# Performance work log

Hardware: AMD Instinct MI355X
Metric: run time of the kernel (lower is better)

The kernel has to match this reference:

```python
import jax, jax.numpy as jnp
import numpy as np

B, L, D_INNER, D_STATE, DT_RANK = 1, 1024, 5120, 16, 160


def setup_inputs() -> dict:
    key = jax.random.key(0)
    k0, k1, k2, k3, k4, k5 = jax.random.split(key, 6)
    x = jax.random.normal(k0, (B, L, D_INNER), dtype=jnp.float32)
    # A_log in [0,1) -> A = -exp(A_log) in [-e,-1]: stable decaying recurrence
    A_log = jax.random.uniform(k1, (D_INNER, D_STATE), dtype=jnp.float32)
    D = jax.random.normal(k2, (D_INNER,), dtype=jnp.float32)
    x_proj_w = jax.random.normal(k3, (DT_RANK + 2 * D_STATE, D_INNER), dtype=jnp.float32) * 0.02
    dt_proj_w = jax.random.normal(k4, (D_INNER, DT_RANK), dtype=jnp.float32) * 0.02
    dt_proj_b = jax.random.normal(k5, (D_INNER,), dtype=jnp.float32) * 0.02
    return {"x": x, "A_log": A_log, "D": D, "x_proj_w": x_proj_w,
            "dt_proj_w": dt_proj_w, "dt_proj_b": dt_proj_b}


def reference(x, A_log, D, x_proj_w, dt_proj_w, dt_proj_b):
    # Mamba ssm(): x (b, l, d_inner) -> y (b, l, d_inner)
    A = -jnp.exp(A_log)                                   # (d, n)
    x_dbl = jnp.einsum('bld,ed->ble', x, x_proj_w)        # (b, l, dt_rank+2n)
    dt = x_dbl[..., :DT_RANK]                             # (b, l, r)
    Bm = x_dbl[..., DT_RANK:DT_RANK + D_STATE]            # (b, l, n)
    Cm = x_dbl[..., DT_RANK + D_STATE:]                   # (b, l, n)
    delta = jax.nn.softplus(jnp.einsum('blr,dr->bld', dt, dt_proj_w) + dt_proj_b)

    # discretization (zero-order hold)
    deltaA = jnp.exp(jnp.einsum('bld,dn->bldn', delta, A))        # (b, l, d, n)
    deltaB_u = jnp.einsum('bld,bln,bld->bldn', delta, Bm, x)      # (b, l, d, n)

    def step(h, inp):
        dA_t, dBu_t, c_t = inp          # (b,d,n), (b,d,n), (b,n)
        h = dA_t * h + dBu_t
        y_t = jnp.einsum('bdn,bn->bd', h, c_t)
        return h, y_t

    h0 = jnp.zeros((x.shape[0], D_INNER, D_STATE), dtype=x.dtype)
    xs = (jnp.swapaxes(deltaA, 0, 1),   # (l, b, d, n)
          jnp.swapaxes(deltaB_u, 0, 1),
          jnp.swapaxes(Cm, 0, 1))
    _, ys = jax.lax.scan(step, h0, xs)  # ys: (l, b, d)
    y = jnp.swapaxes(ys, 0, 1)          # (b, l, d)
    return y + x * D
```

## Files before the change

### kernel.cpp

```cpp
#include <hip/hip_runtime.h>
#include <hip/hip_bf16.h>

#define L_SEQ 1024
#define DI    5120
#define DS    16
#define DR    160
#define NE    192
#define NC    16
#define CL    64
#define SPLITK 8
#define KSPLIT (DI / SPLITK)

#define OFF_P     0
#define SZ_P      (SPLITK * L_SEQ * NE * 4)
#define OFF_XDBL  (OFF_P + SZ_P)
#define SZ_XDBL   (L_SEQ * NE * 4)
#define OFF_DELTA (OFF_XDBL + SZ_XDBL)
#define SZ_DELTA  (L_SEQ * DI * 4)
#define OFF_HEND  (OFF_DELTA + SZ_DELTA)
#define SZ_H      (NC * DS * DI * 4)
#define OFF_APROD (OFF_HEND + SZ_H)
#define OFF_WH    OFF_HEND
#define OFF_WL    (OFF_WH + 1638400)
#define OFF_XH    (OFF_WL + 1638400)
#define OFF_XL    (OFF_XH + 393216)

typedef short s16x8 __attribute__((ext_vector_type(8)));
typedef float f32x4 __attribute__((ext_vector_type(4)));

__device__ __forceinline__ unsigned short bf_rn(float f) {
  unsigned u = __float_as_uint(f);
  u += 0x7FFFu + ((u >> 16) & 1u);
  return (unsigned short)(u >> 16);
}
__device__ __forceinline__ void split_hilo(float f, unsigned short& h, unsigned short& l) {
  h = bf_rn(f);
  float hf = __uint_as_float(((unsigned)h) << 16);
  l = bf_rn(f - hf);
}

__device__ __forceinline__ void load_hilo(const float* __restrict__ p,
                                          s16x8& hi, s16x8& lo) {
  float4 v0 = *(const float4*)p;
  float4 v1 = *(const float4*)(p + 4);
  float f[8] = {v0.x, v0.y, v0.z, v0.w, v1.x, v1.y, v1.z, v1.w};
#pragma unroll
  for (int j = 0; j < 8; ++j) {
    unsigned short h, l;
    split_hilo(f[j], h, l);
    hi[j] = (short)h;
    lo[j] = (short)l;
  }
}

__global__ __launch_bounds__(256) void k_cvt(const float* __restrict__ src,
                                             unsigned short* __restrict__ hi,
                                             unsigned short* __restrict__ lo) {
  int i4 = (blockIdx.x * 256 + threadIdx.x) * 4;
  float4 v = *(const float4*)&src[i4];
  float f[4] = {v.x, v.y, v.z, v.w};
  ushort4 h, l;
  unsigned short hh, ll;
  split_hilo(f[0], hh, ll); h.x = hh; l.x = ll;
  split_hilo(f[1], hh, ll); h.y = hh; l.y = ll;
  split_hilo(f[2], hh, ll); h.z = hh; l.z = ll;
  split_hilo(f[3], hh, ll); h.w = hh; l.w = ll;
  *(ushort4*)&hi[i4] = h;
  *(ushort4*)&lo[i4] = l;
}

__global__ __launch_bounds__(128) void k_xdbl_mfma(const float* __restrict__ x,
                                                   const float* __restrict__ xw,
                                                   float* __restrict__ part) {
  const int lane = threadIdx.x & 63;
  const int w    = threadIdx.x >> 6;
  const int e0   = blockIdx.x * 64 + w * 32;
  const int l0   = blockIdx.y * 32;
  const int kb   = blockIdx.z * KSPLIT;
  const int rc   = lane & 15;
  const int kg   = (lane >> 4) * 8;

  f32x4 acc[2][2] = {};
  for (int k0 = 0; k0 < KSPLIT; k0 += 32) {
    s16x8 ahi[2], alo[2], bhi[2], blo[2];
#pragma unroll
    for (int mf = 0; mf < 2; ++mf)
      load_hilo(&x[(size_t)(l0 + mf * 16 + rc) * DI + kb + k0 + kg], ahi[mf], alo[mf]);
#pragma unroll
    for (int nf = 0; nf < 2; ++nf)
      load_hilo(&xw[(size_t)(e0 + nf * 16 + rc) * DI + kb + k0 + kg], bhi[nf], blo[nf]);
#pragma unroll
    for (int mf = 0; mf < 2; ++mf)
#pragma unroll
      for (int nf = 0; nf < 2; ++nf) {
        acc[mf][nf] = __builtin_amdgcn_mfma_f32_16x16x32_bf16(ahi[mf], bhi[nf], acc[mf][nf], 0, 0, 0);
        acc[mf][nf] = __builtin_amdgcn_mfma_f32_16x16x32_bf16(ahi[mf], blo[nf], acc[mf][nf], 0, 0, 0);
        acc[mf][nf] = __builtin_amdgcn_mfma_f32_16x16x32_bf16(alo[mf], bhi[nf], acc[mf][nf], 0, 0, 0);
      }
  }
#pragma unroll
  for (int mf = 0; mf < 2; ++mf)
#pragma unroll
    for (int nf = 0; nf < 2; ++nf)
#pragma unroll
      for (int r = 0; r < 4; ++r) {
        int l = l0 + mf * 16 + (lane >> 4) * 4 + r;
        int e = e0 + nf * 16 + rc;
        part[((size_t)blockIdx.z * L_SEQ + l) * NE + e] = acc[mf][nf][r];
      }
}

__global__ __launch_bounds__(256) void k_xdbl_reduce(const float* __restrict__ part,
                                                     float* __restrict__ xdbl,
                                                     unsigned short* __restrict__ xh,
                                                     unsigned short* __restrict__ xl) {
  int i4 = (blockIdx.x * 256 + threadIdx.x) * 4;
  float4 s = {0.f, 0.f, 0.f, 0.f};
#pragma unroll
  for (int z = 0; z < SPLITK; ++z) {
    float4 p = *(const float4*)&part[(size_t)z * L_SEQ * NE + i4];
    s.x += p.x; s.y += p.y; s.z += p.z; s.w += p.w;
  }
  *(float4*)&xdbl[i4] = s;
  float f[4] = {s.x, s.y, s.z, s.w};
  ushort4 h, l;
  unsigned short hh, ll;
  split_hilo(f[0], hh, ll); h.x = hh; l.x = ll;
  split_hilo(f[1], hh, ll); h.y = hh; l.y = ll;
  split_hilo(f[2], hh, ll); h.z = hh; l.z = ll;
  split_hilo(f[3], hh, ll); h.w = hh; l.w = ll;
  *(ushort4*)&xh[i4] = h;
  *(ushort4*)&xl[i4] = l;
}

#define AST 168
__global__ __launch_bounds__(512) void k_delta_mfma2(const unsigned short* __restrict__ xh,
                                                     const unsigned short* __restrict__ xl,
                                                     const unsigned short* __restrict__ wh,
                                                     const unsigned short* __restrict__ wlo,
                                                     const float* __restrict__ dtb,
                                                     float* __restrict__ delta) {
  __shared__ unsigned short sAh[64 * AST];
  __shared__ unsigned short sAl[64 * AST];
  const int tid  = threadIdx.x;
  const int lane = tid & 63;
  const int w    = tid >> 6;
  const int wl_  = w >> 2;
  const int wd   = w & 3;
  const int l0   = blockIdx.y * 64;
  const int d0   = blockIdx.x * 128 + wd * 32;
  const int rc   = lane & 15;
  const int kg   = (lane >> 4) * 8;

  for (int idx = tid; idx < 64 * 20; idx += 512) {
    int r = idx / 20, c8 = (idx % 20) * 8;
    *(s16x8*)&sAh[r * AST + c8] = *(const s16x8*)&xh[(size_t)(l0 + r) * NE + c8];
    *(s16x8*)&sAl[r * AST + c8] = *(const s16x8*)&xl[(size_t)(l0 + r) * NE + c8];
  }
  __syncthreads();

  f32x4 acc[2][2] = {};
#pragma unroll
  for (int k0 = 0; k0 < DR; k0 += 32) {
    s16x8 ah[2], al[2], bh[2], bl[2];
#pragma unroll
    for (int mf = 0; mf < 2; ++mf) {
      int row = wl_ * 32 + mf * 16 + rc;
      ah[mf] = *(const s16x8*)&sAh[row * AST + k0 + kg];
      al[mf] = *(const s16x8*)&sAl[row * AST + k0 + kg];
    }
#pragma unroll
    for (int nf = 0; nf < 2; ++nf) {
      size_t d = d0 + nf * 16 + rc;
      bh[nf] = *(const s16x8*)&wh[d * DR + k0 + kg];
      bl[nf] = *(const s16x8*)&wlo[d * DR + k0 + kg];
    }
#pragma unroll
    for (int mf = 0; mf < 2; ++mf)
#pragma unroll
      for (int nf = 0; nf < 2; ++nf) {
        acc[mf][nf] = __builtin_amdgcn_mfma_f32_16x16x32_bf16(ah[mf], bh[nf], acc[mf][nf], 0, 0, 0);
        acc[mf][nf] = __builtin_amdgcn_mfma_f32_16x16x32_bf16(ah[mf], bl[nf], acc[mf][nf], 0, 0, 0);
        acc[mf][nf] = __builtin_amdgcn_mfma_f32_16x16x32_bf16(al[mf], bh[nf], acc[mf][nf], 0, 0, 0);
      }
  }
#pragma unroll
  for (int nf = 0; nf < 2; ++nf) {
    int d = d0 + nf * 16 + rc;
    float bias = dtb[d];
#pragma unroll
    for (int mf = 0; mf < 2; ++mf)
#pragma unroll
      for (int r = 0; r < 4; ++r) {
        int l = l0 + wl_ * 32 + mf * 16 + (lane >> 4) * 4 + r;
        float z = acc[mf][nf][r] + bias;
        float sp = fmaxf(z, 0.f) + __logf(1.f + __expf(-fabsf(z)));
        delta[(size_t)l * DI + d] = sp;
      }
  }
}

__global__ __launch_bounds__(256) void k_scan1(const float* __restrict__ x,
                                               const float* __restrict__ delta,
                                               const float* __restrict__ xdbl,
                                               const float* __restrict__ A_log,
                                               float* __restrict__ hend,
                                               float* __restrict__ aprod) {
  const int lane = threadIdx.x & 63;
  const int w    = threadIdx.x >> 6;
  const int d    = blockIdx.x * 64 + w * 16 + (lane & 15);
  const int ng   = lane >> 4;
  const int c    = blockIdx.y;
  __shared__ __align__(16) float sB[CL][DS];
  for (int i = threadIdx.x; i < CL * DS; i += 256) {
    int t = i >> 4, n = i & 15;
    sB[t][n] = xdbl[(size_t)(c * CL + t) * NE + DR + n];
  }
  __syncthreads();
  float4 av = *(const float4*)&A_log[(size_t)d * DS + ng * 4];
  float a[4] = {-__expf(av.x), -__expf(av.y), -__expf(av.z), -__expf(av.w)};
  float h[4] = {0.f, 0.f, 0.f, 0.f};
  float sdl = 0.f;

  const float* dp = &delta[(size_t)(c * CL) * DI + d];
  const float* xp = &x[(size_t)(c * CL) * DI + d];
  float dl = dp[0], xv = xp[0];
#pragma unroll 4
  for (int tt = 0; tt < CL; ++tt) {
    float dl_n = 0.f, xv_n = 0.f;
    if (tt + 1 < CL) { dl_n = dp[(size_t)(tt + 1) * DI]; xv_n = xp[(size_t)(tt + 1) * DI]; }
    float du = dl * xv;
    sdl += dl;
    float4 b4 = *(const float4*)&sB[tt][ng * 4];
    float bb[4] = {b4.x, b4.y, b4.z, b4.w};
#pragma unroll
    for (int j = 0; j < 4; ++j) {
      float dA = __expf(dl * a[j]);
      h[j] = dA * h[j] + du * bb[j];
    }
    dl = dl_n; xv = xv_n;
  }
#pragma unroll
  for (int j = 0; j < 4; ++j) {
    int n = ng * 4 + j;
    hend[(size_t)(c * DS + n) * DI + d] = h[j];
    aprod[(size_t)(c * DS + n) * DI + d] = __expf(a[j] * sdl);
  }
}

__global__ __launch_bounds__(256) void k_scan2(float* __restrict__ hend,
                                               const float* __restrict__ aprod) {
  int i = blockIdx.x * 256 + threadIdx.x;
  float carry = 0.f;
#pragma unroll
  for (int c = 0; c < NC; ++c) {
    size_t idx = (size_t)c * DS * DI + i;
    float apv = aprod[idx];
    float hv = hend[idx];
    hend[idx] = carry;
    carry = apv * carry + hv;
  }
}

__global__ __launch_bounds__(256) void k_scan3(const float* __restrict__ x,
                                               const float* __restrict__ delta,
                                               const float* __restrict__ xdbl,
                                               const float* __restrict__ A_log,
                                               const float* __restrict__ Dvec,
                                               const float* __restrict__ hstart,
                                               float* __restrict__ out) {
  const int lane = threadIdx.x & 63;
  const int w    = threadIdx.x >> 6;
  const int d    = blockIdx.x * 64 + w * 16 + (lane & 15);
  const int ng   = lane >> 4;
  const int c    = blockIdx.y;
  __shared__ __align__(16) float sB[CL][DS];
  __shared__ __align__(16) float sC[CL][DS];
  for (int i = threadIdx.x; i < CL * DS; i += 256) {
    int t = i >> 4, n = i & 15;
    sB[t][n] = xdbl[(size_t)(c * CL + t) * NE + DR + n];
    sC[t][n] = xdbl[(size_t)(c * CL + t) * NE + DR + DS + n];
  }
  __syncthreads();
  float4 av = *(const float4*)&A_log[(size_t)d * DS + ng * 4];
  float a[4] = {-__expf(av.x), -__expf(av.y), -__expf(av.z), -__expf(av.w)};
  float h[4];
#pragma unroll
  for (int j = 0; j < 4; ++j)
    h[j] = hstart[(size_t)(c * DS + ng * 4 + j) * DI + d];
  const float Dv = Dvec[d];

  const float* dp = &delta[(size_t)(c * CL) * DI + d];
  const float* xp = &x[(size_t)(c * CL) * DI + d];
  float* op = &out[(size_t)(c * CL) * DI + d];
  float dl = dp[0], xv = xp[0];
#pragma unroll 4
  for (int tt = 0; tt < CL; ++tt) {
    float dl_n = 0.f, xv_n = 0.f;
    if (tt + 1 < CL) { dl_n = dp[(size_t)(tt + 1) * DI]; xv_n = xp[(size_t)(tt + 1) * DI]; }
    float du = dl * xv;
    float4 b4 = *(const float4*)&sB[tt][ng * 4];
    float4 c4 = *(const float4*)&sC[tt][ng * 4];
    float bb[4] = {b4.x, b4.y, b4.z, b4.w};
    float cc[4] = {c4.x, c4.y, c4.z, c4.w};
    float y = 0.f;
#pragma unroll
    for (int j = 0; j < 4; ++j) {
      float dA = __expf(dl * a[j]);
      h[j] = dA * h[j] + du * bb[j];
      y += h[j] * cc[j];
    }
    y += __shfl_xor(y, 16, 64);
    y += __shfl_xor(y, 32, 64);
    if (ng == 0) op[(size_t)tt * DI] = fmaf(xv, Dv, y);
    dl = dl_n; xv = xv_n;
  }
}

extern "C" void kernel_launch(void* const* d_in, const int* in_sizes, int n_in,
                              void* d_out, int out_size, void* d_ws, size_t ws_size,
                              hipStream_t stream) {
  const float* x     = (const float*)d_in[0];
  const float* A_log = (const float*)d_in[1];
  const float* Dvec  = (const float*)d_in[2];
  const float* xw    = (const float*)d_in[3];
  const float* dtw   = (const float*)d_in[4];
  const float* dtb   = (const float*)d_in[5];
  float* out = (float*)d_out;

  char* ws = (char*)d_ws;
  float* part  = (float*)(ws + OFF_P);
  float* xdbl  = (float*)(ws + OFF_XDBL);
  float* delta = (float*)(ws + OFF_DELTA);
  float* hend  = (float*)(ws + OFF_HEND);
  float* aprod = (float*)(ws + OFF_APROD);
  unsigned short* wh = (unsigned short*)(ws + OFF_WH);
  unsigned short* wl = (unsigned short*)(ws + OFF_WL);
  unsigned short* xh = (unsigned short*)(ws + OFF_XH);
  unsigned short* xl = (unsigned short*)(ws + OFF_XL);

  k_cvt<<<800, 256, 0, stream>>>(dtw, wh, wl);
  k_xdbl_mfma<<<dim3(3, 32, SPLITK), 128, 0, stream>>>(x, xw, part);
  k_xdbl_reduce<<<192, 256, 0, stream>>>(part, xdbl, xh, xl);
  k_delta_mfma2<<<dim3(40, 16), 512, 0, stream>>>(xh, xl, wh, wl, dtb, delta);
  k_scan1<<<dim3(80, NC), 256, 0, stream>>>(x, delta, xdbl, A_log, hend, aprod);
  k_scan2<<<320, 256, 0, stream>>>(hend, aprod);
  k_scan3<<<dim3(80, NC), 256, 0, stream>>>(x, delta, xdbl, A_log, Dvec, hend, out);
}
```

Measured before the change: 113.8 us.

## Pre-split x and x_proj to bf16 hi/lo, LDS-tile xdbl GEMM, deepen scan prefetch

Adds separate conversion passes that split x and x_proj_w into bf16 hi/lo arrays. The x_dbl GEMM is rewritten to stage A tiles in shared memory, use 64-row blocks and a split-K of 16, so the hi/lo splitting no longer runs inside the GEMM loop and A data is reused across waves. The scan kernels switch to an 8-deep register prefetch buffer for delta and x, and scan2 loads all chunks up front. In exchange it adds an extra full read/write pass over x (about 20MB of bf16 written) and a larger partial-sum buffer for the reduce to read.

New measurement: 107.2 us. -5.8%, faster.

```diff
diff --git a/kernel.cpp b/kernel.cpp
--- a/kernel.cpp
+++ b/kernel.cpp
@@ -8,8 +8,9 @@
 #define NE    192
 #define NC    16
 #define CL    64
-#define SPLITK 8
+#define SPLITK 16
 #define KSPLIT (DI / SPLITK)
+#define BK    64
 
 #define OFF_P     0
 #define SZ_P      (SPLITK * L_SEQ * NE * 4)
@@ -20,10 +21,15 @@
 #define OFF_HEND  (OFF_DELTA + SZ_DELTA)
 #define SZ_H      (NC * DS * DI * 4)
 #define OFF_APROD (OFF_HEND + SZ_H)
+#define WS_END0   (OFF_APROD + SZ_H)
 #define OFF_WH    OFF_HEND
 #define OFF_WL    (OFF_WH + 1638400)
 #define OFF_XH    (OFF_WL + 1638400)
 #define OFF_XL    (OFF_XH + 393216)
+#define OFF_XPH   WS_END0
+#define OFF_XPL   (OFF_XPH + 10485760)
+#define OFF_XWH   (OFF_XPL + 10485760)
+#define OFF_XWL   (OFF_XWH + 1966080)
 
 typedef short s16x8 __attribute__((ext_vector_type(8)));
 typedef float f32x4 __attribute__((ext_vector_type(4)));
@@ -39,24 +45,13 @@
   l = bf_rn(f - hf);
 }
 
-__device__ __forceinline__ void load_hilo(const float* __restrict__ p,
-                                          s16x8& hi, s16x8& lo) {
-  float4 v0 = *(const float4*)p;
-  float4 v1 = *(const float4*)(p + 4);
-  float f[8] = {v0.x, v0.y, v0.z, v0.w, v1.x, v1.y, v1.z, v1.w};
-#pragma unroll
-  for (int j = 0; j < 8; ++j) {
-    unsigned short h, l;
-    split_hilo(f[j], h, l);
-    hi[j] = (short)h;
-    lo[j] = (short)l;
-  }
-}
-
 __global__ __launch_bounds__(256) void k_cvt(const float* __restrict__ src,
                                              unsigned short* __restrict__ hi,
-                                             unsigned short* __restrict__ lo) {
-  int i4 = (blockIdx.x * 256 + threadIdx.x) * 4;
+                                             unsigned short* __restrict__ lo,
+                                             int n4) {
+  int i = blockIdx.x * 256 + threadIdx.x;
+  if (i >= n4) return;
+  int i4 = i * 4;
   float4 v = *(const float4*)&src[i4];
   float f[4] = {v.x, v.y, v.z, v.w};
   ushort4 h, l;
@@ -69,42 +64,66 @@
   *(ushort4*)&lo[i4] = l;
 }
 
-__global__ __launch_bounds__(128) void k_xdbl_mfma(const float* __restrict__ x,
-                                                   const float* __restrict__ xw,
-                                                   float* __restrict__ part) {
-  const int lane = threadIdx.x & 63;
-  const int w    = threadIdx.x >> 6;
-  const int e0   = blockIdx.x * 64 + w * 32;
-  const int l0   = blockIdx.y * 32;
+#define AST2 72
+__global__ __launch_bounds__(256) void k_xdbl_mfma2(const unsigned short* __restrict__ xph,
+                                                    const unsigned short* __restrict__ xpl,
+                                                    const unsigned short* __restrict__ wxh,
+                                                    const unsigned short* __restrict__ wxl,
+                                                    float* __restrict__ part) {
+  __shared__ unsigned short sAh[64 * AST2];
+  __shared__ unsigned short sAl[64 * AST2];
+  const int tid  = threadIdx.x;
+  const int lane = tid & 63;
+  const int w    = tid >> 6;
+  const int wl_  = w >> 1;
+  const int we   = w & 1;
+  const int l0   = blockIdx.y * 64;
+  const int e0   = blockIdx.x * 64 + we * 32;
   const int kb   = blockIdx.z * KSPLIT;
   const int rc   = lane & 15;
   const int kg   = (lane >> 4) * 8;
 
   f32x4 acc[2][2] = {};
-  for (int k0 = 0; k0 < KSPLIT; k0 += 32) {
-    s16x8 ahi[2], alo[2], bhi[2], blo[2];
-#pragma unroll
-    for (int mf = 0; mf < 2; ++mf)
-      load_hilo(&x[(size_t)(l0 + mf * 16 + rc) * DI + kb + k0 + kg], ahi[mf], alo[mf]);
+  for (int k0 = 0; k0 < KSPLIT; k0 += BK) {
+    __syncthreads();
+    for (int idx = tid; idx < 64 * 8; idx += 256) {
+      int r = idx >> 3, c8 = (idx & 7) * 8;
+      *(s16x8*)&sAh[r * AST2 + c8] = *(const s16x8*)&xph[(size_t)(l0 + r) * DI + kb + k0 + c8];
+      *(s16x8*)&sAl[r * AST2 + c8] = *(const s16x8*)&xpl[(size_t)(l0 + r) * DI + kb + k0 + c8];
+    }
+    __syncthreads();
+#pragma unroll
+    for (int ks = 0; ks < BK; ks += 32) {
+      s16x8 ah[2], al[2], bh[2], bl[2];
+#pragma unroll
+      for (int mf = 0; mf < 2; ++mf) {
+        int row = wl_ * 32 + mf * 16 + rc;
+        ah[mf] = *(const s16x8*)&sAh[row * AST2 + ks + kg];
+        al[mf] = *(const s16x8*)&sAl[row * AST2 + ks + kg];
+      }
+#pragma unroll
+      for (int nf = 0; nf < 2; ++nf) {
+        size_t e = e0 + nf * 16 + rc;
+        bh[nf] = *(const s16x8*)&wxh[e * DI + kb + k0 + ks + kg];
+        bl[nf] = *(const s16x8*)&wxl[e * DI + kb + k0 + ks + kg];
+      }
+#pragma unroll
+      for (int mf = 0; mf < 2; ++mf)
+#pragma unroll
+        for (int nf = 0; nf < 2; ++nf) {
+          acc[mf][nf] = __builtin_amdgcn_mfma_f32_16x16x32_bf16(ah[mf], bh[nf], acc[mf][nf], 0, 0, 0);
+          acc[mf][nf] = __builtin_amdgcn_mfma_f32_16x16x32_bf16(ah[mf], bl[nf], acc[mf][nf], 0, 0, 0);
+          acc[mf][nf] = __builtin_amdgcn_mfma_f32_16x16x32_bf16(al[mf], bh[nf], acc[mf][nf], 0, 0, 0);
+        }
+    }
+  }
+#pragma unroll
+  for (int mf = 0; mf < 2; ++mf)
 #pragma unroll
     for (int nf = 0; nf < 2; ++nf)
-      load_hilo(&xw[(size_t)(e0 + nf * 16 + rc) * DI + kb + k0 + kg], bhi[nf], blo[nf]);
-#pragma unroll
-    for (int mf = 0; mf < 2; ++mf)
-#pragma unroll
-      for (int nf = 0; nf < 2; ++nf) {
-        acc[mf][nf] = __builtin_amdgcn_mfma_f32_16x16x32_bf16(ahi[mf], bhi[nf], acc[mf][nf], 0, 0, 0);
-        acc[mf][nf] = __builtin_amdgcn_mfma_f32_16x16x32_bf16(ahi[mf], blo[nf], acc[mf][nf], 0, 0, 0);
-        acc[mf][nf] = __builtin_amdgcn_mfma_f32_16x16x32_bf16(alo[mf], bhi[nf], acc[mf][nf], 0, 0, 0);
-      }
-  }
-#pragma unroll
-  for (int mf = 0; mf < 2; ++mf)
-#pragma unroll
-    for (int nf = 0; nf < 2; ++nf)
 #pragma unroll
       for (int r = 0; r < 4; ++r) {
-        int l = l0 + mf * 16 + (lane >> 4) * 4 + r;
+        int l = l0 + wl_ * 32 + mf * 16 + (lane >> 4) * 4 + r;
         int e = e0 + nf * 16 + rc;
         part[((size_t)blockIdx.z * L_SEQ + l) * NE + e] = acc[mf][nf][r];
       }
@@ -224,41 +243,50 @@
 
   const float* dp = &delta[(size_t)(c * CL) * DI + d];
   const float* xp = &x[(size_t)(c * CL) * DI + d];
-  float dl = dp[0], xv = xp[0];
-#pragma unroll 4
-  for (int tt = 0; tt < CL; ++tt) {
-    float dl_n = 0.f, xv_n = 0.f;
-    if (tt + 1 < CL) { dl_n = dp[(size_t)(tt + 1) * DI]; xv_n = xp[(size_t)(tt + 1) * DI]; }
-    float du = dl * xv;
-    sdl += dl;
-    float4 b4 = *(const float4*)&sB[tt][ng * 4];
-    float bb[4] = {b4.x, b4.y, b4.z, b4.w};
-#pragma unroll
-    for (int j = 0; j < 4; ++j) {
-      float dA = __expf(dl * a[j]);
-      h[j] = dA * h[j] + du * bb[j];
-    }
-    dl = dl_n; xv = xv_n;
-  }
-#pragma unroll
-  for (int j = 0; j < 4; ++j) {
-    int n = ng * 4 + j;
-    hend[(size_t)(c * DS + n) * DI + d] = h[j];
-    aprod[(size_t)(c * DS + n) * DI + d] = __expf(a[j] * sdl);
+  float dlb[8], xvb[8];
+#pragma unroll
+  for (int j = 0; j < 8; ++j) { dlb[j] = dp[(size_t)j * DI]; xvb[j] = xp[(size_t)j * DI]; }
+  for (int tt = 0; tt < CL; tt += 8) {
+#pragma unroll
+    for (int j = 0; j < 8; ++j) {
+      float dl = dlb[j], xv = xvb[j];
+      int tn = tt + 8 + j;
+      if (tn < CL) { dlb[j] = dp[(size_t)tn * DI]; xvb[j] = xp[(size_t)tn * DI]; }
+      float du = dl * xv;
+      sdl += dl;
+      float4 b4 = *(const float4*)&sB[tt + j][ng * 4];
+      float bb[4] = {b4.x, b4.y, b4.z, b4.w};
+#pragma unroll
+      for (int q = 0; q < 4; ++q) {
+        float dA = __expf(dl * a[q]);
+        h[q] = dA * h[q] + du * bb[q];
+      }
+    }
+  }
+#pragma unroll
+  for (int q = 0; q < 4; ++q) {
+    int n = ng * 4 + q;
+    hend[(size_t)(c * DS + n) * DI + d] = h[q];
+    aprod[(size_t)(c * DS + n) * DI + d] = __expf(a[q] * sdl);
   }
 }
 
 __global__ __launch_bounds__(256) void k_scan2(float* __restrict__ hend,
                                                const float* __restrict__ aprod) {
   int i = blockIdx.x * 256 + threadIdx.x;
-  float carry = 0.f;
+  float ap[NC], hv[NC];
 #pragma unroll
   for (int c = 0; c < NC; ++c) {
     size_t idx = (size_t)c * DS * DI + i;
-    float apv = aprod[idx];
-    float hv = hend[idx];
+    ap[c] = aprod[idx];
+    hv[c] = hend[idx];
+  }
+  float carry = 0.f;
+#pragma unroll
+  for (int c = 0; c < NC; ++c) {
+    size_t idx = (size_t)c * DS * DI + i;
     hend[idx] = carry;
-    carry = apv * carry + hv;
+    carry = ap[c] * carry + hv[c];
   }
 }
 
@@ -286,34 +314,38 @@
   float a[4] = {-__expf(av.x), -__expf(av.y), -__expf(av.z), -__expf(av.w)};
   float h[4];
 #pragma unroll
-  for (int j = 0; j < 4; ++j)
-    h[j] = hstart[(size_t)(c * DS + ng * 4 + j) * DI + d];
+  for (int q = 0; q < 4; ++q)
+    h[q] = hstart[(size_t)(c * DS + ng * 4 + q) * DI + d];
   const float Dv = Dvec[d];
 
   const float* dp = &delta[(size_t)(c * CL) * DI + d];
   const float* xp = &x[(size_t)(c * CL) * DI + d];
   float* op = &out[(size_t)(c * CL) * DI + d];
-  float dl = dp[0], xv = xp[0];
-#pragma unroll 4
-  for (int tt = 0; tt < CL; ++tt) {
-    float dl_n = 0.f, xv_n = 0.f;
-    if (tt + 1 < CL) { dl_n = dp[(size_t)(tt + 1) * DI]; xv_n = xp[(size_t)(tt + 1) * DI]; }
-    float du = dl * xv;
-    float4 b4 = *(const float4*)&sB[tt][ng * 4];
-    float4 c4 = *(const float4*)&sC[tt][ng * 4];
-    float bb[4] = {b4.x, b4.y, b4.z, b4.w};
-    float cc[4] = {c4.x, c4.y, c4.z, c4.w};
-    float y = 0.f;
-#pragma unroll
-    for (int j = 0; j < 4; ++j) {
-      float dA = __expf(dl * a[j]);
-      h[j] = dA * h[j] + du * bb[j];
-      y += h[j] * cc[j];
-    }
-    y += __shfl_xor(y, 16, 64);
-    y += __shfl_xor(y, 32, 64);
-    if (ng == 0) op[(size_t)tt * DI] = fmaf(xv, Dv, y);
-    dl = dl_n; xv = xv_n;
+  float dlb[8], xvb[8];
+#pragma unroll
+  for (int j = 0; j < 8; ++j) { dlb[j] = dp[(size_t)j * DI]; xvb[j] = xp[(size_t)j * DI]; }
+  for (int tt = 0; tt < CL; tt += 8) {
+#pragma unroll
+    for (int j = 0; j < 8; ++j) {
+      float dl = dlb[j], xv = xvb[j];
+      int tn = tt + 8 + j;
+      if (tn < CL) { dlb[j] = dp[(size_t)tn * DI]; xvb[j] = xp[(size_t)tn * DI]; }
+      float du = dl * xv;
+      float4 b4 = *(const float4*)&sB[tt + j][ng * 4];
+      float4 c4 = *(const float4*)&sC[tt + j][ng * 4];
+      float bb[4] = {b4.x, b4.y, b4.z, b4.w};
+      float cc[4] = {c4.x, c4.y, c4.z, c4.w};
+      float y = 0.f;
+#pragma unroll
+      for (int q = 0; q < 4; ++q) {
+        float dA = __expf(dl * a[q]);
+        h[q] = dA * h[q] + du * bb[q];
+        y += h[q] * cc[q];
+      }
+      y += __shfl_xor(y, 16, 64);
+      y += __shfl_xor(y, 32, 64);
+      if (ng == 0) op[(size_t)(tt + j) * DI] = fmaf(xv, Dv, y);
+    }
   }
 }
 
@@ -334,13 +366,19 @@
   float* delta = (float*)(ws + OFF_DELTA);
   float* hend  = (float*)(ws + OFF_HEND);
   float* aprod = (float*)(ws + OFF_APROD);
-  unsigned short* wh = (unsigned short*)(ws + OFF_WH);
-  unsigned short* wl = (unsigned short*)(ws + OFF_WL);
-  unsigned short* xh = (unsigned short*)(ws + OFF_XH);
-  unsigned short* xl = (unsigned short*)(ws + OFF_XL);
-
-  k_cvt<<<800, 256, 0, stream>>>(dtw, wh, wl);
-  k_xdbl_mfma<<<dim3(3, 32, SPLITK), 128, 0, stream>>>(x, xw, part);
+  unsigned short* wh  = (unsigned short*)(ws + OFF_WH);
+  unsigned short* wl  = (unsigned short*)(ws + OFF_WL);
+  unsigned short* xh  = (unsigned short*)(ws + OFF_XH);
+  unsigned short* xl  = (unsigned short*)(ws + OFF_XL);
+  unsigned short* xph = (unsigned short*)(ws + OFF_XPH);
+  unsigned short* xpl = (unsigned short*)(ws + OFF_XPL);
+  unsigned short* wxh = (unsigned short*)(ws + OFF_XWH);
+  unsigned short* wxl = (unsigned short*)(ws + OFF_XWL);
+
+  k_cvt<<<5120, 256, 0, stream>>>(x, xph, xpl, L_SEQ * DI / 4);
+  k_cvt<<<960, 256, 0, stream>>>(xw, wxh, wxl, NE * DI / 4);
+  k_cvt<<<800, 256, 0, stream>>>(dtw, wh, wl, DI * DR / 4);
+  k_xdbl_mfma2<<<dim3(3, 16, SPLITK), 256, 0, stream>>>(xph, xpl, wxh, wxl, part);
   k_xdbl_reduce<<<192, 256, 0, stream>>>(part, xdbl, xh, xl);
   k_delta_mfma2<<<dim3(40, 16), 512, 0, stream>>>(xh, xl, wh, wl, dtb, delta);
   k_scan1<<<dim3(80, NC), 256, 0, stream>>>(x, delta, xdbl, A_log, hend, aprod);
```
